# Kernel optimization log

Measured on AMD Instinct MI355X. Metric: run time of the kernel, lower is better.

Reference implementation:

```python
import jax, jax.numpy as jnp
import numpy as np

B, L, H_IN = 2, 512, 768
E = 256          # hidden_size
N = 12           # num_labels


def setup_inputs() -> dict:
    key = jax.random.key(0)
    ks = jax.random.split(key, 10)
    lim_in = 1.0 / np.sqrt(H_IN)
    lim_e = 1.0 / np.sqrt(E)
    lim_2e = 1.0 / np.sqrt(2 * E)
    return {
        "x":    jax.random.normal(ks[0], (B, L, H_IN), dtype=jnp.float32),
        "sW":   jax.random.uniform(ks[1], (E, H_IN), jnp.float32, -lim_in, lim_in),
        "sb":   jax.random.uniform(ks[2], (E,), jnp.float32, -lim_in, lim_in),
        "tW":   jax.random.uniform(ks[3], (E, H_IN), jnp.float32, -lim_in, lim_in),
        "tb":   jax.random.uniform(ks[4], (E,), jnp.float32, -lim_in, lim_in),
        "f2W":  jax.random.uniform(ks[5], (E, 2 * E), jnp.float32, -lim_2e, lim_2e),
        "f2b":  jax.random.uniform(ks[6], (E,), jnp.float32, -lim_2e, lim_2e),
        "f3W":  jax.random.normal(ks[7], (N, E), dtype=jnp.float32),  # init_weights: normal_
        "f3b":  jax.random.uniform(ks[8], (N,), jnp.float32, -lim_e, lim_e),
        "blW":  jax.random.normal(ks[9], (E * N, E), dtype=jnp.float32),  # bi_linear, no bias
    }


def reference(x, sW, sb, tW, tb, f2W, f2b, f3W, f3b, blW):
    b, l, _ = x.shape
    s = jax.nn.relu(x @ sW.T + sb)  # [B,L,E]
    t = jax.nn.relu(x @ tW.T + tb)  # [B,L,E]
    # biaffine term: key[b,s,e,n] = (s @ blW.T) reshaped, then key @ t^T
    key = (s @ blW.T).reshape(b, l, E, N)             # [B,L,E,N]
    out1 = jnp.einsum('bsen,ble->bsnl', key, t)       # [B,S,N,L]
    # pairwise concat-MLP, decomposed: cat(u,v) @ f2W.T == u@Wu.T + v@Wv.T
    Wu, Wv = f2W[:, :E], f2W[:, E:]
    su = s @ Wu.T                                     # [B,L,E]
    tv = t @ Wv.T                                     # [B,L,E]
    h = jax.nn.relu(su[:, :, None, :] + tv[:, None, :, :] + f2b)  # [B,L,L,E]
    out2 = h @ f3W.T + f3b                            # [B,L,L,N]
    out2 = jnp.transpose(out2, (0, 1, 3, 2))          # [B,L,N,L]
    return out1 + out2
```

## Files before the change

kernel.cpp:

```cpp
#include <hip/hip_runtime.h>
#include <hip/hip_bf16.h>


typedef unsigned short u16;
typedef __attribute__((ext_vector_type(8))) short    s16x8;
typedef __attribute__((ext_vector_type(8))) _Float16 f16x8;
typedef __attribute__((ext_vector_type(4))) float    f32x4;

__device__ inline u16 f2h(float f) { return __builtin_bit_cast(u16, (_Float16)f); }

__device__ inline f32x4 mfma_f16(s16x8 a, s16x8 b, f32x4 c) {
    return __builtin_amdgcn_mfma_f32_16x16x32_f16(
        __builtin_bit_cast(f16x8, a), __builtin_bit_cast(f16x8, b), c, 0, 0, 0);
}
__device__ inline f32x4 mfma_f16v(f16x8 a, s16x8 b, f32x4 c) {
    return __builtin_amdgcn_mfma_f32_16x16x32_f16(a, __builtin_bit_cast(f16x8, b), c, 0, 0, 0);
}

__global__ __launch_bounds__(256)
void conv_kernel(const float* __restrict__ x, const float* __restrict__ sW,
                 const float* __restrict__ tW, const float* __restrict__ sb,
                 const float* __restrict__ tb, const float* __restrict__ f2W,
                 const float* __restrict__ blW, const float* __restrict__ f3W,
                 u16* __restrict__ xb, u16* __restrict__ wstb, float* __restrict__ sbtb,
                 u16* __restrict__ blkw, u16* __restrict__ f2wvb, u16* __restrict__ f3wb)
{
    int idx = blockIdx.x * 256 + threadIdx.x;
    if (idx >= 525440) return;
    float4 v;
    u16* dst;
    if (idx < 196608) {
        v = *(const float4*)&x[idx * 4];
        dst = &xb[idx * 4];
    } else if (idx < 294912) {
        int i4 = (idx - 196608) * 4;
        int row = i4 / 768, k = i4 - row * 768;
        const float* src = (row < 256) ? &sW[row * 768 + k] : &tW[(row - 256) * 768 + k];
        v = *(const float4*)src;
        dst = &wstb[i4];
    } else if (idx < 295040) {
        int i4 = (idx - 294912) * 4;
        float4 s = (i4 < 256) ? *(const float4*)&sb[i4] : *(const float4*)&tb[i4 - 256];
        *(float4*)&sbtb[i4] = s;
        return;
    } else if (idx < 508032) {
        int i4 = (idx - 295040) * 4;
        int r = i4 >> 8, k = i4 & 255;
        const float* src;
        if (r < 3072) { int n = r >> 8, e = r & 255; src = &blW[(e * 12 + n) * 256 + k]; }
        else           { src = &f2W[(r - 3072) * 512 + k]; }
        v = *(const float4*)src;
        dst = &blkw[i4];
    } else if (idx < 524416) {
        int i4 = (idx - 508032) * 4;
        int e = i4 >> 8, k = i4 & 255;
        v = *(const float4*)&f2W[e * 512 + 256 + k];
        dst = &f2wvb[i4];
    } else {
        int i4 = (idx - 524416) * 4;
        int row = i4 >> 8, e = i4 & 255;
        if (row < 12) v = *(const float4*)&f3W[row * 256 + e];
        else          v = make_float4(0.f, 0.f, 0.f, 0.f);
        dst = &f3wb[i4];
    }
    ushort4 o;
    o.x = f2h(v.x); o.y = f2h(v.y); o.z = f2h(v.z); o.w = f2h(v.w);
    *(ushort4*)dst = o;
}

template<int MODE>
__global__ __launch_bounds__(256, 2)
void gemm_mfma(const u16* __restrict__ A, int lda,
               const u16* __restrict__ BT, int ldb,
               const float* __restrict__ bias,
               void* __restrict__ out0, void* __restrict__ out1p, int K)
{
    __shared__ u16 As[64 * 72];
    __shared__ u16 Bs[64 * 72];
    const int tid = threadIdx.x;
    const int m0 = blockIdx.y * 64, n0 = blockIdx.x * 64;
    const int w = tid >> 6, l = tid & 63;
    const int wr = (w >> 1) * 32, wc = (w & 1) * 32;
    const int lr = l & 15, lg = l >> 4;
    const int srow = tid >> 2, kq = tid & 3;

    const u16* ap = &A [(size_t)(m0 + srow) * lda];
    const u16* bp = &BT[(size_t)(n0 + srow) * ldb];
    s16x8 ra0 = *(const s16x8*)&ap[kq * 8];
    s16x8 ra1 = *(const s16x8*)&ap[(kq + 4) * 8];
    s16x8 rb0 = *(const s16x8*)&bp[kq * 8];
    s16x8 rb1 = *(const s16x8*)&bp[(kq + 4) * 8];

    f32x4 acc[2][2] = {};
    for (int k0 = 0; k0 < K; k0 += 64) {
        __syncthreads();
        *(s16x8*)&As[srow * 72 + kq * 8]       = ra0;
        *(s16x8*)&As[srow * 72 + (kq + 4) * 8] = ra1;
        *(s16x8*)&Bs[srow * 72 + kq * 8]       = rb0;
        *(s16x8*)&Bs[srow * 72 + (kq + 4) * 8] = rb1;
        __syncthreads();
        if (k0 + 64 < K) {
            ra0 = *(const s16x8*)&ap[k0 + 64 + kq * 8];
            ra1 = *(const s16x8*)&ap[k0 + 64 + (kq + 4) * 8];
            rb0 = *(const s16x8*)&bp[k0 + 64 + kq * 8];
            rb1 = *(const s16x8*)&bp[k0 + 64 + (kq + 4) * 8];
        }
#pragma unroll
        for (int kk = 0; kk < 64; kk += 32) {
            s16x8 af[2], bf[2];
            af[0] = *(const s16x8*)&As[(wr      + lr) * 72 + kk + lg * 8];
            af[1] = *(const s16x8*)&As[(wr + 16 + lr) * 72 + kk + lg * 8];
            bf[0] = *(const s16x8*)&Bs[(wc      + lr) * 72 + kk + lg * 8];
            bf[1] = *(const s16x8*)&Bs[(wc + 16 + lr) * 72 + kk + lg * 8];
#pragma unroll
            for (int fi = 0; fi < 2; ++fi)
#pragma unroll
                for (int fj = 0; fj < 2; ++fj)
                    acc[fi][fj] = mfma_f16(af[fi], bf[fj], acc[fi][fj]);
        }
    }
#pragma unroll
    for (int fi = 0; fi < 2; ++fi) {
#pragma unroll
        for (int fj = 0; fj < 2; ++fj) {
#pragma unroll
            for (int r = 0; r < 4; ++r) {
                int grow = m0 + wr + fi * 16 + lg * 4 + r;
                int gcol = n0 + wc + fj * 16 + lr;
                float v = acc[fi][fj][r];
                if (MODE == 0) {
                    v = fmaxf(v + bias[gcol], 0.f);
                    ((u16*)out0)[(size_t)grow * 512 + gcol] = f2h(v);
                } else if (MODE == 1) {
                    if (gcol < 3072) {
                        int n = gcol >> 8, e = gcol & 255;
                        ((u16*)out0)[(size_t)n * 262144 + (size_t)grow * 256 + e] = f2h(v);
                    } else {
                        ((u16*)out1p)[(size_t)grow * 256 + (gcol - 3072)] = f2h(v);
                    }
                } else {
                    ((u16*)out0)[(size_t)grow * 256 + gcol] = f2h(v + bias[gcol]);
                }
            }
        }
    }
}

__global__ __launch_bounds__(256, 4)
void fused_out(const u16* __restrict__ KEYP, const u16* __restrict__ STb,
               const u16* __restrict__ SUh, const u16* __restrict__ TVh,
               const u16* __restrict__ F3WH, const float* __restrict__ f3b,
               float* __restrict__ out)
{
    __shared__ __align__(16) char smem[30208];
    u16* lds = (u16*)smem;
    const int KEYC = 0, TC = 7680, SUC = 8960, TVC = 9600, F3C = 10880;

    const int tid = threadIdx.x;
    const int w = tid >> 6, l = tid & 63;
    const int b  = blockIdx.z;
    const int i0 = blockIdx.y * 16;
    const int j0 = blockIdx.x * 32;
    const int lr = l & 15, lg = l >> 4;

    const u16* sb_[5]; int do_[5];
#pragma unroll
    for (int rr = 0; rr < 5; ++rr) {
        int g = tid + 256 * rr;
        const u16* s = nullptr; int d = 0;
        if (g < 768) {
            int n = g >> 6, ii = (g >> 2) & 15, qq = g & 3;
            s = KEYP + (size_t)n * 262144 + (size_t)(b * 512 + i0 + ii) * 256 + qq * 8;
            d = KEYC + (n * 16 + ii) * 40 + qq * 8;
        } else if (g < 896) {
            int q = g - 768, jj = q >> 2, qq = q & 3;
            s = STb + (size_t)(b * 512 + j0 + jj) * 512 + 256 + qq * 8;
            d = TC + jj * 40 + qq * 8;
        } else if (g < 960) {
            int q = g - 896, ii = q >> 2, qq = q & 3;
            s = SUh + (size_t)(b * 512 + i0 + ii) * 256 + qq * 8;
            d = SUC + ii * 40 + qq * 8;
        } else {
            int q = g - 960, jj = q >> 2, qq = q & 3;
            s = TVh + (size_t)(b * 512 + j0 + jj) * 256 + qq * 8;
            d = TVC + jj * 40 + qq * 8;
        }
        sb_[rr] = s; do_[rr] = d;
    }
    const bool v4 = (tid < 64);

#pragma unroll
    for (int rr = 0; rr < 2; ++rr) {
        int g = tid + 256 * rr;
        int row = g >> 5, qq = g & 31;
        *(s16x8*)&lds[F3C + row * 264 + qq * 8] = *(const s16x8*)&F3WH[row * 256 + qq * 8];
    }

    s16x8 st0, st1, st2, st3, st4 = {};
    f32x4 acc1[3][2] = {};
    f32x4 acc2[8]    = {};

    st0 = *(const s16x8*)(sb_[0]);
    st1 = *(const s16x8*)(sb_[1]);
    st2 = *(const s16x8*)(sb_[2]);
    st3 = *(const s16x8*)(sb_[3]);
    if (v4) st4 = *(const s16x8*)(sb_[4]);

    for (int it = 0; it < 8; ++it) {
        const int e0 = it * 32;
        __syncthreads();
        *(s16x8*)&lds[do_[0]] = st0;
        *(s16x8*)&lds[do_[1]] = st1;
        *(s16x8*)&lds[do_[2]] = st2;
        *(s16x8*)&lds[do_[3]] = st3;
        if (v4) *(s16x8*)&lds[do_[4]] = st4;
        __syncthreads();
        if (it < 7) {
            st0 = *(const s16x8*)(sb_[0] + e0 + 32);
            st1 = *(const s16x8*)(sb_[1] + e0 + 32);
            st2 = *(const s16x8*)(sb_[2] + e0 + 32);
            st3 = *(const s16x8*)(sb_[3] + e0 + 32);
            if (v4) st4 = *(const s16x8*)(sb_[4] + e0 + 32);
        }
        s16x8 tf0 = *(const s16x8*)&lds[TC + lr * 40 + lg * 8];
        s16x8 tf1 = *(const s16x8*)&lds[TC + (16 + lr) * 40 + lg * 8];
#pragma unroll
        for (int a = 0; a < 3; ++a) {
            int n = 3 * w + a;
            s16x8 kf = *(const s16x8*)&lds[KEYC + (n * 16 + lr) * 40 + lg * 8];
            acc1[a][0] = mfma_f16(kf, tf0, acc1[a][0]);
            acc1[a][1] = mfma_f16(kf, tf1, acc1[a][1]);
        }
        f16x8 sv = __builtin_bit_cast(f16x8, *(const s16x8*)&lds[SUC + lr * 40 + lg * 8]);
        s16x8 f3fr = *(const s16x8*)&lds[F3C + lr * 264 + e0 + lg * 8];
#pragma unroll
        for (int jj = 0; jj < 8; ++jj) {
            int j = w * 8 + jj;
            f16x8 tv8 = __builtin_bit_cast(f16x8, *(const s16x8*)&lds[TVC + j * 40 + lg * 8]);
            f16x8 hv = sv + tv8;
#pragma unroll
            for (int q = 0; q < 8; ++q)
                hv[q] = hv[q] > (_Float16)0.f ? hv[q] : (_Float16)0.f;
            acc2[jj] = mfma_f16v(hv, f3fr, acc2[jj]);
        }
    }

    __syncthreads();
    float* mg = (float*)smem;
    if (lr < 12) {
#pragma unroll
        for (int r = 0; r < 4; ++r) {
            int i = lg * 4 + r;
            f32x4 v0, v1;
            v0[0] = acc2[0][r]; v0[1] = acc2[1][r]; v0[2] = acc2[2][r]; v0[3] = acc2[3][r];
            v1[0] = acc2[4][r]; v1[1] = acc2[5][r]; v1[2] = acc2[6][r]; v1[3] = acc2[7][r];
            *(f32x4*)&mg[lr * 580 + i * 36 + w * 8]     = v0;
            *(f32x4*)&mg[lr * 580 + i * 36 + w * 8 + 4] = v1;
        }
    }
    __syncthreads();
#pragma unroll
    for (int a = 0; a < 3; ++a) {
        int n = 3 * w + a;
        float fb = f3b[n];
#pragma unroll
        for (int fj = 0; fj < 2; ++fj) {
            int j = fj * 16 + lr;
#pragma unroll
            for (int r = 0; r < 4; ++r) {
                int i = lg * 4 + r;
                float vv = acc1[a][fj][r] + mg[n * 580 + i * 36 + j] + fb;
                out[(((size_t)(b * 512 + i0 + i)) * 12 + n) * 512 + j0 + j] = vv;
            }
        }
    }
}

extern "C" void kernel_launch(void* const* d_in, const int* in_sizes, int n_in,
                              void* d_out, int out_size, void* d_ws, size_t ws_size,
                              hipStream_t stream)
{
    const float* x   = (const float*)d_in[0];
    const float* sW  = (const float*)d_in[1];
    const float* sb  = (const float*)d_in[2];
    const float* tW  = (const float*)d_in[3];
    const float* tb  = (const float*)d_in[4];
    const float* f2W = (const float*)d_in[5];
    const float* f2b = (const float*)d_in[6];
    const float* f3W = (const float*)d_in[7];
    const float* f3b = (const float*)d_in[8];
    const float* blW = (const float*)d_in[9];
    float* out = (float*)d_out;

    char* p = (char*)d_ws;
    u16*   xb    = (u16*)p;   p += 1572864;
    u16*   wstb  = (u16*)p;   p += 786432;
    float* sbtb  = (float*)p; p += 2048;
    u16*   STb   = (u16*)p;   p += 1048576;
    u16*   blkw  = (u16*)p;   p += 1703936;
    u16*   KEYP  = (u16*)p;   p += 6291456;
    u16*   SUp   = (u16*)p;   p += 524288;
    u16*   f2wvb = (u16*)p;   p += 131072;
    u16*   TVp   = (u16*)p;   p += 524288;
    u16*   f3wbg = (u16*)p;   p += 8192;

    conv_kernel<<<2053, 256, 0, stream>>>(x, sW, tW, sb, tb, f2W, blW, f3W,
                                          xb, wstb, sbtb, blkw, f2wvb, f3wbg);
    gemm_mfma<0><<<dim3(8, 16),  256, 0, stream>>>(xb, 768, wstb, 768, sbtb, STb, nullptr, 768);
    gemm_mfma<1><<<dim3(52, 16), 256, 0, stream>>>(STb, 512, blkw, 256, nullptr, KEYP, SUp, 256);
    gemm_mfma<2><<<dim3(4, 16),  256, 0, stream>>>(STb + 256, 512, f2wvb, 256, f2b, TVp, nullptr, 256);
    fused_out<<<dim3(16, 32, 2), 256, 0, stream>>>(KEYP, STb, SUp, TVp, f3wbg, f3b, out);
}
```

Baseline: 52.53 us.

## Fuse fp32->fp16 conversion into first GEMM, merge TV GEMM, load KEY/TV directly to registers

The first GEMM now reads fp32 x and sW/tW directly and converts to fp16 while staging into shared memory, so the separate conversion pass over x and the weights is dropped. The TV projection is merged into the KEY/SU GEMM launch by appending its weights to the combined weight matrix and choosing the A offset per column block, which removes one launch. In the fused output kernel, KEY and TV fragments are loaded straight from global memory into registers instead of through LDS, which shrinks shared memory and adds register pressure (launch bounds lowered to 3 blocks per SM).

```diff
diff --git a/kernel.cpp b/kernel.cpp
--- a/kernel.cpp
+++ b/kernel.cpp
@@ -9,6 +9,13 @@
 
 __device__ inline u16 f2h(float f) { return __builtin_bit_cast(u16, (_Float16)f); }
 
+__device__ inline s16x8 cvt2(float4 a, float4 b) {
+    f16x8 h;
+    h[0] = (_Float16)a.x; h[1] = (_Float16)a.y; h[2] = (_Float16)a.z; h[3] = (_Float16)a.w;
+    h[4] = (_Float16)b.x; h[5] = (_Float16)b.y; h[6] = (_Float16)b.z; h[7] = (_Float16)b.w;
+    return __builtin_bit_cast(s16x8, h);
+}
+
 __device__ inline f32x4 mfma_f16(s16x8 a, s16x8 b, f32x4 c) {
     return __builtin_amdgcn_mfma_f32_16x16x32_f16(
         __builtin_bit_cast(f16x8, a), __builtin_bit_cast(f16x8, b), c, 0, 0, 0);
@@ -18,46 +25,25 @@
 }
 
 __global__ __launch_bounds__(256)
-void conv_kernel(const float* __restrict__ x, const float* __restrict__ sW,
-                 const float* __restrict__ tW, const float* __restrict__ sb,
-                 const float* __restrict__ tb, const float* __restrict__ f2W,
-                 const float* __restrict__ blW, const float* __restrict__ f3W,
-                 u16* __restrict__ xb, u16* __restrict__ wstb, float* __restrict__ sbtb,
-                 u16* __restrict__ blkw, u16* __restrict__ f2wvb, u16* __restrict__ f3wb)
+void conv_kernel(const float* __restrict__ f2W, const float* __restrict__ blW,
+                 const float* __restrict__ f3W,
+                 u16* __restrict__ blkw, u16* __restrict__ f3wb)
 {
     int idx = blockIdx.x * 256 + threadIdx.x;
-    if (idx >= 525440) return;
+    if (idx >= 230400) return;
     float4 v;
     u16* dst;
-    if (idx < 196608) {
-        v = *(const float4*)&x[idx * 4];
-        dst = &xb[idx * 4];
-    } else if (idx < 294912) {
-        int i4 = (idx - 196608) * 4;
-        int row = i4 / 768, k = i4 - row * 768;
-        const float* src = (row < 256) ? &sW[row * 768 + k] : &tW[(row - 256) * 768 + k];
-        v = *(const float4*)src;
-        dst = &wstb[i4];
-    } else if (idx < 295040) {
-        int i4 = (idx - 294912) * 4;
-        float4 s = (i4 < 256) ? *(const float4*)&sb[i4] : *(const float4*)&tb[i4 - 256];
-        *(float4*)&sbtb[i4] = s;
-        return;
-    } else if (idx < 508032) {
-        int i4 = (idx - 295040) * 4;
+    if (idx < 229376) {
+        int i4 = idx * 4;
         int r = i4 >> 8, k = i4 & 255;
         const float* src;
-        if (r < 3072) { int n = r >> 8, e = r & 255; src = &blW[(e * 12 + n) * 256 + k]; }
-        else           { src = &f2W[(r - 3072) * 512 + k]; }
+        if (r < 3072)      { int n = r >> 8, e = r & 255; src = &blW[(e * 12 + n) * 256 + k]; }
+        else if (r < 3328) { src = &f2W[(r - 3072) * 512 + k]; }
+        else               { src = &f2W[(r - 3328) * 512 + 256 + k]; }
         v = *(const float4*)src;
         dst = &blkw[i4];
-    } else if (idx < 524416) {
-        int i4 = (idx - 508032) * 4;
-        int e = i4 >> 8, k = i4 & 255;
-        v = *(const float4*)&f2W[e * 512 + 256 + k];
-        dst = &f2wvb[i4];
     } else {
-        int i4 = (idx - 524416) * 4;
+        int i4 = (idx - 229376) * 4;
         int row = i4 >> 8, e = i4 & 255;
         if (row < 12) v = *(const float4*)&f3W[row * 256 + e];
         else          v = make_float4(0.f, 0.f, 0.f, 0.f);
@@ -68,12 +54,10 @@
     *(ushort4*)dst = o;
 }
 
-template<int MODE>
 __global__ __launch_bounds__(256, 2)
-void gemm_mfma(const u16* __restrict__ A, int lda,
-               const u16* __restrict__ BT, int ldb,
-               const float* __restrict__ bias,
-               void* __restrict__ out0, void* __restrict__ out1p, int K)
+void gemm_st(const float* __restrict__ x, const float* __restrict__ sW,
+             const float* __restrict__ tW, const float* __restrict__ sb,
+             const float* __restrict__ tb, u16* __restrict__ STb)
 {
     __shared__ u16 As[64 * 72];
     __shared__ u16 Bs[64 * 72];
@@ -84,26 +68,28 @@
     const int lr = l & 15, lg = l >> 4;
     const int srow = tid >> 2, kq = tid & 3;
 
-    const u16* ap = &A [(size_t)(m0 + srow) * lda];
-    const u16* bp = &BT[(size_t)(n0 + srow) * ldb];
-    s16x8 ra0 = *(const s16x8*)&ap[kq * 8];
-    s16x8 ra1 = *(const s16x8*)&ap[(kq + 4) * 8];
-    s16x8 rb0 = *(const s16x8*)&bp[kq * 8];
-    s16x8 rb1 = *(const s16x8*)&bp[(kq + 4) * 8];
+    const float* ap = &x[(size_t)(m0 + srow) * 768 + kq * 16];
+    int brow = n0 + srow;
+    const float* bp = (brow < 256) ? &sW[(size_t)brow * 768 + kq * 16]
+                                   : &tW[(size_t)(brow - 256) * 768 + kq * 16];
+    float4 ra0 = *(const float4*)(ap + 0),  ra1 = *(const float4*)(ap + 4);
+    float4 ra2 = *(const float4*)(ap + 8),  ra3 = *(const float4*)(ap + 12);
+    float4 rb0 = *(const float4*)(bp + 0),  rb1 = *(const float4*)(bp + 4);
+    float4 rb2 = *(const float4*)(bp + 8),  rb3 = *(const float4*)(bp + 12);
 
     f32x4 acc[2][2] = {};
-    for (int k0 = 0; k0 < K; k0 += 64) {
-        __syncthreads();
-        *(s16x8*)&As[srow * 72 + kq * 8]       = ra0;
-        *(s16x8*)&As[srow * 72 + (kq + 4) * 8] = ra1;
-        *(s16x8*)&Bs[srow * 72 + kq * 8]       = rb0;
-        *(s16x8*)&Bs[srow * 72 + (kq + 4) * 8] = rb1;
-        __syncthreads();
-        if (k0 + 64 < K) {
-            ra0 = *(const s16x8*)&ap[k0 + 64 + kq * 8];
-            ra1 = *(const s16x8*)&ap[k0 + 64 + (kq + 4) * 8];
-            rb0 = *(const s16x8*)&bp[k0 + 64 + kq * 8];
-            rb1 = *(const s16x8*)&bp[k0 + 64 + (kq + 4) * 8];
+    for (int k0 = 0; k0 < 768; k0 += 64) {
+        __syncthreads();
+        *(s16x8*)&As[srow * 72 + kq * 16]     = cvt2(ra0, ra1);
+        *(s16x8*)&As[srow * 72 + kq * 16 + 8] = cvt2(ra2, ra3);
+        *(s16x8*)&Bs[srow * 72 + kq * 16]     = cvt2(rb0, rb1);
+        *(s16x8*)&Bs[srow * 72 + kq * 16 + 8] = cvt2(rb2, rb3);
+        __syncthreads();
+        if (k0 + 64 < 768) {
+            ra0 = *(const float4*)(ap + k0 + 64 + 0);  ra1 = *(const float4*)(ap + k0 + 64 + 4);
+            ra2 = *(const float4*)(ap + k0 + 64 + 8);  ra3 = *(const float4*)(ap + k0 + 64 + 12);
+            rb0 = *(const float4*)(bp + k0 + 64 + 0);  rb1 = *(const float4*)(bp + k0 + 64 + 4);
+            rb2 = *(const float4*)(bp + k0 + 64 + 8);  rb3 = *(const float4*)(bp + k0 + 64 + 12);
         }
 #pragma unroll
         for (int kk = 0; kk < 64; kk += 32) {
@@ -127,34 +113,95 @@
             for (int r = 0; r < 4; ++r) {
                 int grow = m0 + wr + fi * 16 + lg * 4 + r;
                 int gcol = n0 + wc + fj * 16 + lr;
+                float bias = (gcol < 256) ? sb[gcol] : tb[gcol - 256];
+                float v = fmaxf(acc[fi][fj][r] + bias, 0.f);
+                STb[(size_t)grow * 512 + gcol] = f2h(v);
+            }
+        }
+    }
+}
+
+__global__ __launch_bounds__(256, 2)
+void gemm_kst(const u16* __restrict__ STb, const u16* __restrict__ BLKW,
+              const float* __restrict__ f2b,
+              u16* __restrict__ KEYP, u16* __restrict__ SUp, u16* __restrict__ TVp)
+{
+    __shared__ u16 As[64 * 72];
+    __shared__ u16 Bs[64 * 72];
+    const int tid = threadIdx.x;
+    const int m0 = blockIdx.y * 64, n0 = blockIdx.x * 64;
+    const int w = tid >> 6, l = tid & 63;
+    const int wr = (w >> 1) * 32, wc = (w & 1) * 32;
+    const int lr = l & 15, lg = l >> 4;
+    const int srow = tid >> 2, kq = tid & 3;
+
+    const u16* A = STb + (n0 >= 3328 ? 256 : 0);
+    const u16* ap = &A[(size_t)(m0 + srow) * 512];
+    const u16* bp = &BLKW[(size_t)(n0 + srow) * 256];
+    s16x8 ra0 = *(const s16x8*)&ap[kq * 8];
+    s16x8 ra1 = *(const s16x8*)&ap[(kq + 4) * 8];
+    s16x8 rb0 = *(const s16x8*)&bp[kq * 8];
+    s16x8 rb1 = *(const s16x8*)&bp[(kq + 4) * 8];
+
+    f32x4 acc[2][2] = {};
+    for (int k0 = 0; k0 < 256; k0 += 64) {
+        __syncthreads();
+        *(s16x8*)&As[srow * 72 + kq * 8]       = ra0;
+        *(s16x8*)&As[srow * 72 + (kq + 4) * 8] = ra1;
+        *(s16x8*)&Bs[srow * 72 + kq * 8]       = rb0;
+        *(s16x8*)&Bs[srow * 72 + (kq + 4) * 8] = rb1;
+        __syncthreads();
+        if (k0 + 64 < 256) {
+            ra0 = *(const s16x8*)&ap[k0 + 64 + kq * 8];
+            ra1 = *(const s16x8*)&ap[k0 + 64 + (kq + 4) * 8];
+            rb0 = *(const s16x8*)&bp[k0 + 64 + kq * 8];
+            rb1 = *(const s16x8*)&bp[k0 + 64 + (kq + 4) * 8];
+        }
+#pragma unroll
+        for (int kk = 0; kk < 64; kk += 32) {
+            s16x8 af[2], bf[2];
+            af[0] = *(const s16x8*)&As[(wr      + lr) * 72 + kk + lg * 8];
+            af[1] = *(const s16x8*)&As[(wr + 16 + lr) * 72 + kk + lg * 8];
+            bf[0] = *(const s16x8*)&Bs[(wc      + lr) * 72 + kk + lg * 8];
+            bf[1] = *(const s16x8*)&Bs[(wc + 16 + lr) * 72 + kk + lg * 8];
+#pragma unroll
+            for (int fi = 0; fi < 2; ++fi)
+#pragma unroll
+                for (int fj = 0; fj < 2; ++fj)
+                    acc[fi][fj] = mfma_f16(af[fi], bf[fj], acc[fi][fj]);
+        }
+    }
+#pragma unroll
+    for (int fi = 0; fi < 2; ++fi) {
+#pragma unroll
+        for (int fj = 0; fj < 2; ++fj) {
+#pragma unroll
+            for (int r = 0; r < 4; ++r) {
+                int grow = m0 + wr + fi * 16 + lg * 4 + r;
+                int gcol = n0 + wc + fj * 16 + lr;
                 float v = acc[fi][fj][r];
-                if (MODE == 0) {
-                    v = fmaxf(v + bias[gcol], 0.f);
-                    ((u16*)out0)[(size_t)grow * 512 + gcol] = f2h(v);
-                } else if (MODE == 1) {
-                    if (gcol < 3072) {
-                        int n = gcol >> 8, e = gcol & 255;
-                        ((u16*)out0)[(size_t)n * 262144 + (size_t)grow * 256 + e] = f2h(v);
-                    } else {
-                        ((u16*)out1p)[(size_t)grow * 256 + (gcol - 3072)] = f2h(v);
-                    }
+                if (gcol < 3072) {
+                    int n = gcol >> 8, e = gcol & 255;
+                    KEYP[(size_t)n * 262144 + (size_t)grow * 256 + e] = f2h(v);
+                } else if (gcol < 3328) {
+                    SUp[(size_t)grow * 256 + (gcol - 3072)] = f2h(v);
                 } else {
-                    ((u16*)out0)[(size_t)grow * 256 + gcol] = f2h(v + bias[gcol]);
+                    TVp[(size_t)grow * 256 + (gcol - 3328)] = f2h(v + f2b[gcol - 3328]);
                 }
             }
         }
     }
 }
 
-__global__ __launch_bounds__(256, 4)
+__global__ __launch_bounds__(256, 3)
 void fused_out(const u16* __restrict__ KEYP, const u16* __restrict__ STb,
-               const u16* __restrict__ SUh, const u16* __restrict__ TVh,
+               const u16* __restrict__ SUp, const u16* __restrict__ TVp,
                const u16* __restrict__ F3WH, const float* __restrict__ f3b,
                float* __restrict__ out)
 {
-    __shared__ __align__(16) char smem[30208];
+    __shared__ __align__(16) char smem[27904];
     u16* lds = (u16*)smem;
-    const int KEYC = 0, TC = 7680, SUC = 8960, TVC = 9600, F3C = 10880;
+    const int TC = 0, SUC = 1280, F3C = 1920;
 
     const int tid = threadIdx.x;
     const int w = tid >> 6, l = tid & 63;
@@ -163,31 +210,17 @@
     const int j0 = blockIdx.x * 32;
     const int lr = l & 15, lg = l >> 4;
 
-    const u16* sb_[5]; int do_[5];
-#pragma unroll
-    for (int rr = 0; rr < 5; ++rr) {
-        int g = tid + 256 * rr;
-        const u16* s = nullptr; int d = 0;
-        if (g < 768) {
-            int n = g >> 6, ii = (g >> 2) & 15, qq = g & 3;
-            s = KEYP + (size_t)n * 262144 + (size_t)(b * 512 + i0 + ii) * 256 + qq * 8;
-            d = KEYC + (n * 16 + ii) * 40 + qq * 8;
-        } else if (g < 896) {
-            int q = g - 768, jj = q >> 2, qq = q & 3;
-            s = STb + (size_t)(b * 512 + j0 + jj) * 512 + 256 + qq * 8;
-            d = TC + jj * 40 + qq * 8;
-        } else if (g < 960) {
-            int q = g - 896, ii = q >> 2, qq = q & 3;
-            s = SUh + (size_t)(b * 512 + i0 + ii) * 256 + qq * 8;
-            d = SUC + ii * 40 + qq * 8;
-        } else {
-            int q = g - 960, jj = q >> 2, qq = q & 3;
-            s = TVh + (size_t)(b * 512 + j0 + jj) * 256 + qq * 8;
-            d = TVC + jj * 40 + qq * 8;
-        }
-        sb_[rr] = s; do_[rr] = d;
-    }
-    const bool v4 = (tid < 64);
+    const u16* ssrc = nullptr; int sdst = 0;
+    if (tid < 128) {
+        int jj = tid >> 2, qq = tid & 3;
+        ssrc = STb + (size_t)(b * 512 + j0 + jj) * 512 + 256 + qq * 8;
+        sdst = TC + jj * 40 + qq * 8;
+    } else if (tid < 192) {
+        int q = tid - 128, ii = q >> 2, qq = q & 3;
+        ssrc = SUp + (size_t)(b * 512 + i0 + ii) * 256 + qq * 8;
+        sdst = SUC + ii * 40 + qq * 8;
+    }
+    const bool stg = (tid < 192);
 
 #pragma unroll
     for (int rr = 0; rr < 2; ++rr) {
@@ -196,52 +229,57 @@
         *(s16x8*)&lds[F3C + row * 264 + qq * 8] = *(const s16x8*)&F3WH[row * 256 + qq * 8];
     }
 
-    s16x8 st0, st1, st2, st3, st4 = {};
+    const u16* kp0 = KEYP + (size_t)(3 * w + 0) * 262144 + (size_t)(b * 512 + i0 + lr) * 256 + lg * 8;
+    const u16* kp1 = kp0 + 262144;
+    const u16* kp2 = kp1 + 262144;
+    const u16* tvp = TVp + (size_t)(b * 512 + j0 + w * 8) * 256 + lg * 8;
+
+    s16x8 st = {};
+    if (stg) st = *(const s16x8*)ssrc;
+    s16x8 kf0 = *(const s16x8*)kp0;
+    s16x8 kf1 = *(const s16x8*)kp1;
+    s16x8 kf2 = *(const s16x8*)kp2;
+    s16x8 tv[8];
+#pragma unroll
+    for (int jj = 0; jj < 8; ++jj) tv[jj] = *(const s16x8*)(tvp + jj * 256);
+
     f32x4 acc1[3][2] = {};
     f32x4 acc2[8]    = {};
 
-    st0 = *(const s16x8*)(sb_[0]);
-    st1 = *(const s16x8*)(sb_[1]);
-    st2 = *(const s16x8*)(sb_[2]);
-    st3 = *(const s16x8*)(sb_[3]);
-    if (v4) st4 = *(const s16x8*)(sb_[4]);
-
     for (int it = 0; it < 8; ++it) {
         const int e0 = it * 32;
         __syncthreads();
-        *(s16x8*)&lds[do_[0]] = st0;
-        *(s16x8*)&lds[do_[1]] = st1;
-        *(s16x8*)&lds[do_[2]] = st2;
-        *(s16x8*)&lds[do_[3]] = st3;
-        if (v4) *(s16x8*)&lds[do_[4]] = st4;
-        __syncthreads();
-        if (it < 7) {
-            st0 = *(const s16x8*)(sb_[0] + e0 + 32);
-            st1 = *(const s16x8*)(sb_[1] + e0 + 32);
-            st2 = *(const s16x8*)(sb_[2] + e0 + 32);
-            st3 = *(const s16x8*)(sb_[3] + e0 + 32);
-            if (v4) st4 = *(const s16x8*)(sb_[4] + e0 + 32);
-        }
+        if (stg) *(s16x8*)&lds[sdst] = st;
+        __syncthreads();
+        if (it < 7 && stg) st = *(const s16x8*)(ssrc + e0 + 32);
+
         s16x8 tf0 = *(const s16x8*)&lds[TC + lr * 40 + lg * 8];
         s16x8 tf1 = *(const s16x8*)&lds[TC + (16 + lr) * 40 + lg * 8];
-#pragma unroll
-        for (int a = 0; a < 3; ++a) {
-            int n = 3 * w + a;
-            s16x8 kf = *(const s16x8*)&lds[KEYC + (n * 16 + lr) * 40 + lg * 8];
-            acc1[a][0] = mfma_f16(kf, tf0, acc1[a][0]);
-            acc1[a][1] = mfma_f16(kf, tf1, acc1[a][1]);
-        }
+        acc1[0][0] = mfma_f16(kf0, tf0, acc1[0][0]);
+        acc1[0][1] = mfma_f16(kf0, tf1, acc1[0][1]);
+        acc1[1][0] = mfma_f16(kf1, tf0, acc1[1][0]);
+        acc1[1][1] = mfma_f16(kf1, tf1, acc1[1][1]);
+        acc1[2][0] = mfma_f16(kf2, tf0, acc1[2][0]);
+        acc1[2][1] = mfma_f16(kf2, tf1, acc1[2][1]);
+
         f16x8 sv = __builtin_bit_cast(f16x8, *(const s16x8*)&lds[SUC + lr * 40 + lg * 8]);
         s16x8 f3fr = *(const s16x8*)&lds[F3C + lr * 264 + e0 + lg * 8];
 #pragma unroll
         for (int jj = 0; jj < 8; ++jj) {
-            int j = w * 8 + jj;
-            f16x8 tv8 = __builtin_bit_cast(f16x8, *(const s16x8*)&lds[TVC + j * 40 + lg * 8]);
-            f16x8 hv = sv + tv8;
+            f16x8 hv = sv + __builtin_bit_cast(f16x8, tv[jj]);
 #pragma unroll
             for (int q = 0; q < 8; ++q)
                 hv[q] = hv[q] > (_Float16)0.f ? hv[q] : (_Float16)0.f;
             acc2[jj] = mfma_f16v(hv, f3fr, acc2[jj]);
+        }
+
+        if (it < 7) {
+            int off = e0 + 32;
+            kf0 = *(const s16x8*)(kp0 + off);
+            kf1 = *(const s16x8*)(kp1 + off);
+            kf2 = *(const s16x8*)(kp2 + off);
+#pragma unroll
+            for (int jj = 0; jj < 8; ++jj) tv[jj] = *(const s16x8*)(tvp + jj * 256 + off);
         }
     }
 
@@ -293,21 +331,15 @@
     float* out = (float*)d_out;
 
     char* p = (char*)d_ws;
-    u16*   xb    = (u16*)p;   p += 1572864;
-    u16*   wstb  = (u16*)p;   p += 786432;
-    float* sbtb  = (float*)p; p += 2048;
-    u16*   STb   = (u16*)p;   p += 1048576;
-    u16*   blkw  = (u16*)p;   p += 1703936;
-    u16*   KEYP  = (u16*)p;   p += 6291456;
-    u16*   SUp   = (u16*)p;   p += 524288;
-    u16*   f2wvb = (u16*)p;   p += 131072;
-    u16*   TVp   = (u16*)p;   p += 524288;
-    u16*   f3wbg = (u16*)p;   p += 8192;
-
-    conv_kernel<<<2053, 256, 0, stream>>>(x, sW, tW, sb, tb, f2W, blW, f3W,
-                                          xb, wstb, sbtb, blkw, f2wvb, f3wbg);
-    gemm_mfma<0><<<dim3(8, 16),  256, 0, stream>>>(xb, 768, wstb, 768, sbtb, STb, nullptr, 768);
-    gemm_mfma<1><<<dim3(52, 16), 256, 0, stream>>>(STb, 512, blkw, 256, nullptr, KEYP, SUp, 256);
-    gemm_mfma<2><<<dim3(4, 16),  256, 0, stream>>>(STb + 256, 512, f2wvb, 256, f2b, TVp, nullptr, 256);
+    u16* STb   = (u16*)p; p += 1048576;
+    u16* blkw  = (u16*)p; p += 1835008;
+    u16* KEYP  = (u16*)p; p += 6291456;
+    u16* SUp   = (u16*)p; p += 524288;
+    u16* TVp   = (u16*)p; p += 524288;
+    u16* f3wbg = (u16*)p; p += 8192;
+
+    conv_kernel<<<900, 256, 0, stream>>>(f2W, blW, f3W, blkw, f3wbg);
+    gemm_st <<<dim3(8, 16),  256, 0, stream>>>(x, sW, tW, sb, tb, STb);
+    gemm_kst<<<dim3(56, 16), 256, 0, stream>>>(STb, blkw, f2b, KEYP, SUp, TVp);
     fused_out<<<dim3(16, 32, 2), 256, 0, stream>>>(KEYP, STb, SUp, TVp, f3wbg, f3b, out);
 }
```

New measurement: 56.80 us. +8.1%, slower.
